# Optimization experiments

Measured on AMD Instinct MI355X. Metric: run time of the kernel, lower is better.

## Reference

```python
import jax, jax.numpy as jnp
import numpy as np

N = 8192
F_IN = 128
F_OUT = 64
NEG_INF = -9e15


def setup_inputs() -> dict:
    key = jax.random.key(0)
    k1, k2, k3, k4 = jax.random.split(key, 4)
    x = jax.random.normal(k1, (N, F_IN), dtype=jnp.float32)
    adj = jax.random.randint(k2, (N, N), 0, 2, dtype=jnp.int32)
    W = jax.random.normal(k3, (F_OUT, F_IN), dtype=jnp.float32) * 0.05  # torch Linear weight [out,in]
    a = jax.random.normal(k4, (1, 2 * F_OUT), dtype=jnp.float32) * 0.05  # attention vector weight [1, 2*out]
    return {"x": x, "adj": adj, "W": W, "a": a}


def reference(x, adj, W, a):
    fout = W.shape[0]
    Wh = x @ W.T                                   # [N, out]
    a1 = a[0, :fout]                               # a.weight.T[:out]
    a2 = a[0, fout:]                               # a.weight.T[out:]
    Wh1 = Wh @ a1                                  # [N]
    Wh2 = Wh @ a2                                  # [N]
    e = jax.nn.leaky_relu(Wh1[:, None] + Wh2[None, :], negative_slope=0.2)  # [N, N]
    attention = jnp.where(adj > 0, e, NEG_INF)
    attention = jax.nn.softmax(attention, axis=1)
    # dropout is identity in eval / deterministic reference
    h_prime = attention @ Wh                       # [N, out]
    return jax.nn.elu(h_prime)
```

## Files before the change

### kernel.cpp

```cpp
#include <hip/hip_runtime.h>
#include <cstdint>
#include <cstddef>

#define NN 8192
#define FIN 128
#define FOUT 64

typedef __attribute__((ext_vector_type(8))) short short8;
typedef __attribute__((ext_vector_type(4))) float f32x4;

__device__ __forceinline__ unsigned short f32_to_bf16_bits(float f) {
    union { float f; uint32_t u; } c; c.f = f;
    uint32_t u = c.u;
    u += 0x7fffu + ((u >> 16) & 1u);
    return (unsigned short)(u >> 16);
}

__device__ __forceinline__ unsigned int pack_bf16(float lo, float hi) {
    return (unsigned int)f32_to_bf16_bits(lo) |
           ((unsigned int)f32_to_bf16_bits(hi) << 16);
}

__global__ __launch_bounds__(256) void gat_prep(
    const float* __restrict__ x, const float* __restrict__ W,
    const float* __restrict__ a, unsigned short* __restrict__ WhT,
    float* __restrict__ Wh1, float* __restrict__ Wh2)
{
    const int t    = threadIdx.x;
    const int f    = t & 63;
    const int iloc = t >> 6;
    const int i    = blockIdx.x * 4 + iloc;

    const float4* x4 = (const float4*)(x + (size_t)i * FIN);
    const float4* w4 = (const float4*)(W + (size_t)f * FIN);

    float acc = 0.f;
#pragma unroll
    for (int k = 0; k < FIN / 4; ++k) {
        float4 xv = x4[k];
        float4 wv = w4[k];
        acc += xv.x * wv.x + xv.y * wv.y + xv.z * wv.z + xv.w * wv.w;
    }

    WhT[(size_t)f * NN + i] = f32_to_bf16_bits(acc);

    float r1 = acc * a[f];
    float r2 = acc * a[64 + f];
#pragma unroll
    for (int m = 1; m < 64; m <<= 1) {
        r1 += __shfl_xor(r1, m, 64);
        r2 += __shfl_xor(r2, m, 64);
    }
    if (f == 0) { Wh1[i] = r1; Wh2[i] = r2; }
}

__global__ __launch_bounds__(256, 4) void gat_attn(
    const int* __restrict__ adj, const unsigned short* __restrict__ WhT,
    const float* __restrict__ Wh1, const float* __restrict__ Wh2,
    float* __restrict__ Cpart, float* __restrict__ Tpart)
{
    __shared__ float lds_C[4][16][68];
    __shared__ float lds_tot[4][16];

    const int tid  = threadIdx.x;
    const int wave = tid >> 6;
    const int lane = tid & 63;
    const int il   = lane & 15;
    const int q    = lane >> 4;
    const int rt   = blockIdx.x >> 1;
    const int jh   = blockIdx.x & 1;
    const int i0   = rt * 16;
    const int i    = i0 + il;

    const float wh1   = Wh1[i];
    const int   jbase = jh * 4096 + wave * 32 + q * 8;
    const int* __restrict__ adjrow = adj + (size_t)i * NN;

    const short8* bp0 = (const short8*)(WhT + (size_t)(0  + il) * NN);
    const short8* bp1 = (const short8*)(WhT + (size_t)(16 + il) * NN);
    const short8* bp2 = (const short8*)(WhT + (size_t)(32 + il) * NN);
    const short8* bp3 = (const short8*)(WhT + (size_t)(48 + il) * NN);

    f32x4 acc0 = {0.f, 0.f, 0.f, 0.f};
    f32x4 acc1 = {0.f, 0.f, 0.f, 0.f};
    f32x4 acc2 = {0.f, 0.f, 0.f, 0.f};
    f32x4 acc3 = {0.f, 0.f, 0.f, 0.f};
    float tot = 0.f;

    int4   av0 = *(const int4*)(adjrow + jbase);
    int4   av1 = *(const int4*)(adjrow + jbase + 4);
    float4 w20 = *(const float4*)(Wh2 + jbase);
    float4 w21 = *(const float4*)(Wh2 + jbase + 4);
    int jb = jbase >> 3;
    short8 b0 = bp0[jb];
    short8 b1 = bp1[jb];
    short8 b2 = bp2[jb];
    short8 b3 = bp3[jb];

    for (int tt = 0; tt < 32; ++tt) {
        const int jn = jbase + (((tt + 1) & 31) << 7);
        const int4   nav0 = *(const int4*)(adjrow + jn);
        const int4   nav1 = *(const int4*)(adjrow + jn + 4);
        const float4 nw20 = *(const float4*)(Wh2 + jn);
        const float4 nw21 = *(const float4*)(Wh2 + jn + 4);
        const int jnb = jn >> 3;
        const short8 nb0 = bp0[jnb];
        const short8 nb1 = bp1[jnb];
        const short8 nb2 = bp2[jnb];
        const short8 nb3 = bp3[jnb];

        float wv[8];
#define CALC(idx, adjv, wh2v)                                          \
        {                                                              \
            float s = wh1 + (wh2v);                                    \
            float e = fmaxf(s, 0.2f * s);          \
            float v = ((adjv) > 0) ? __expf(e) : 0.f;                  \
            tot += v;                                                  \
            wv[idx] = v;                                               \
        }
        CALC(0, av0.x, w20.x) CALC(1, av0.y, w20.y)
        CALC(2, av0.z, w20.z) CALC(3, av0.w, w20.w)
        CALC(4, av1.x, w21.x) CALC(5, av1.y, w21.y)
        CALC(6, av1.z, w21.z) CALC(7, av1.w, w21.w)
#undef CALC

        union { short8 v; unsigned int u[4]; } af;
        af.u[0] = pack_bf16(wv[0], wv[1]);
        af.u[1] = pack_bf16(wv[2], wv[3]);
        af.u[2] = pack_bf16(wv[4], wv[5]);
        af.u[3] = pack_bf16(wv[6], wv[7]);

        acc0 = __builtin_amdgcn_mfma_f32_16x16x32_bf16(af.v, b0, acc0, 0, 0, 0);
        acc1 = __builtin_amdgcn_mfma_f32_16x16x32_bf16(af.v, b1, acc1, 0, 0, 0);
        acc2 = __builtin_amdgcn_mfma_f32_16x16x32_bf16(af.v, b2, acc2, 0, 0, 0);
        acc3 = __builtin_amdgcn_mfma_f32_16x16x32_bf16(af.v, b3, acc3, 0, 0, 0);

        av0 = nav0; av1 = nav1; w20 = nw20; w21 = nw21;
        b0 = nb0; b1 = nb1; b2 = nb2; b3 = nb3;
    }

    tot += __shfl_xor(tot, 16, 64);
    tot += __shfl_xor(tot, 32, 64);
    if (lane < 16) lds_tot[wave][lane] = tot;

#pragma unroll
    for (int r = 0; r < 4; ++r) {
        lds_C[wave][q * 4 + r][0 * 16 + il] = acc0[r];
        lds_C[wave][q * 4 + r][1 * 16 + il] = acc1[r];
        lds_C[wave][q * 4 + r][2 * 16 + il] = acc2[r];
        lds_C[wave][q * 4 + r][3 * 16 + il] = acc3[r];
    }
    __syncthreads();

#pragma unroll
    for (int e = 0; e < 4; ++e) {
        const int idx = e * 256 + tid;
        const int ii = idx >> 6;
        const int ff = idx & 63;
        float s = lds_C[0][ii][ff] + lds_C[1][ii][ff] +
                  lds_C[2][ii][ff] + lds_C[3][ii][ff];
        Cpart[((size_t)jh * NN + i0 + ii) * FOUT + ff] = s;
        if (ff == 0) {
            float ts = lds_tot[0][ii] + lds_tot[1][ii] +
                       lds_tot[2][ii] + lds_tot[3][ii];
            Tpart[(size_t)jh * NN + i0 + ii] = ts;
        }
    }
}

__global__ __launch_bounds__(256) void gat_combine(
    const float* __restrict__ Cpart, const float* __restrict__ Tpart,
    float* __restrict__ out)
{
    const int idx = blockIdx.x * 256 + threadIdx.x;
    const int i = idx >> 6;
    const float c = Cpart[idx] + Cpart[(size_t)NN * FOUT + idx];
    const float t = Tpart[i] + Tpart[NN + i];
    const float p = c / t;
    out[idx] = (p > 0.f) ? p : (__expf(p) - 1.f);
}

extern "C" void kernel_launch(void* const* d_in, const int* in_sizes, int n_in,
                              void* d_out, int out_size, void* d_ws, size_t ws_size,
                              hipStream_t stream) {
    const float* x   = (const float*)d_in[0];
    const int*   adj = (const int*)d_in[1];
    const float* W   = (const float*)d_in[2];
    const float* a   = (const float*)d_in[3];
    float* out = (float*)d_out;

    char* ws = (char*)d_ws;
    unsigned short* WhT = (unsigned short*)ws;
    float* Wh1   = (float*)(ws + (size_t)1048576);
    float* Wh2   = (float*)(ws + (size_t)1048576 + 32768);
    float* Cpart = (float*)(ws + (size_t)2097152);
    float* Tpart = (float*)(ws + (size_t)6291456);

    gat_prep<<<dim3(NN / 4), dim3(256), 0, stream>>>(x, W, a, WhT, Wh1, Wh2);
    gat_attn<<<dim3(NN / 16 * 2), dim3(256), 0, stream>>>(adj, WhT, Wh1, Wh2, Cpart, Tpart);
    gat_combine<<<dim3(NN * FOUT / 256), dim3(256), 0, stream>>>(Cpart, Tpart, out);
}
```

Baseline: 424.4 us.

## Fuse combine into attention kernel with 512-thread blocks and deeper adj prefetch

The attention kernel now uses 8 waves per 16-row tile covering the full neighbour range instead of splitting the j range across two blocks. This removes the partial-sum buffers and the separate combine kernel, since normalisation and ELU are applied in the epilogue. It also prefetches adj and Wh2 two iterations ahead, loads the WhT operands inside the iteration without prefetch, splits the running sum into two accumulators, and uses the HIP bf16 pack intrinsic. There are half as many blocks as before (512 of 512 threads), which lowers the parallelism available to hide adj memory latency on the dominant 256 MB read.

```diff
diff --git a/kernel.cpp b/kernel.cpp
--- a/kernel.cpp
+++ b/kernel.cpp
@@ -1,4 +1,5 @@
 #include <hip/hip_runtime.h>
+#include <hip/hip_bf16.h>
 #include <cstdint>
 #include <cstddef>
 
@@ -14,11 +15,6 @@
     uint32_t u = c.u;
     u += 0x7fffu + ((u >> 16) & 1u);
     return (unsigned short)(u >> 16);
-}
-
-__device__ __forceinline__ unsigned int pack_bf16(float lo, float hi) {
-    return (unsigned int)f32_to_bf16_bits(lo) |
-           ((unsigned int)f32_to_bf16_bits(hi) << 16);
 }
 
 __global__ __launch_bounds__(256) void gat_prep(
@@ -54,26 +50,24 @@
     if (f == 0) { Wh1[i] = r1; Wh2[i] = r2; }
 }
 
-__global__ __launch_bounds__(256, 4) void gat_attn(
+__global__ __launch_bounds__(512, 4) void gat_attn(
     const int* __restrict__ adj, const unsigned short* __restrict__ WhT,
     const float* __restrict__ Wh1, const float* __restrict__ Wh2,
-    float* __restrict__ Cpart, float* __restrict__ Tpart)
+    float* __restrict__ out)
 {
-    __shared__ float lds_C[4][16][68];
-    __shared__ float lds_tot[4][16];
+    __shared__ float lds_C[8][16][68];
+    __shared__ float lds_tot[8][16];
 
     const int tid  = threadIdx.x;
     const int wave = tid >> 6;
     const int lane = tid & 63;
     const int il   = lane & 15;
     const int q    = lane >> 4;
-    const int rt   = blockIdx.x >> 1;
-    const int jh   = blockIdx.x & 1;
-    const int i0   = rt * 16;
+    const int i0   = blockIdx.x * 16;
     const int i    = i0 + il;
 
     const float wh1   = Wh1[i];
-    const int   jbase = jh * 4096 + wave * 32 + q * 8;
+    const int   jbase = wave * 32 + q * 8;
     const int* __restrict__ adjrow = adj + (size_t)i * NN;
 
     const short8* bp0 = (const short8*)(WhT + (size_t)(0  + il) * NN);
@@ -85,60 +79,62 @@
     f32x4 acc1 = {0.f, 0.f, 0.f, 0.f};
     f32x4 acc2 = {0.f, 0.f, 0.f, 0.f};
     f32x4 acc3 = {0.f, 0.f, 0.f, 0.f};
-    float tot = 0.f;
+    float tot0 = 0.f, tot1 = 0.f;
 
-    int4   av0 = *(const int4*)(adjrow + jbase);
-    int4   av1 = *(const int4*)(adjrow + jbase + 4);
-    float4 w20 = *(const float4*)(Wh2 + jbase);
-    float4 w21 = *(const float4*)(Wh2 + jbase + 4);
-    int jb = jbase >> 3;
-    short8 b0 = bp0[jb];
-    short8 b1 = bp1[jb];
-    short8 b2 = bp2[jb];
-    short8 b3 = bp3[jb];
+    int4   aA0 = *(const int4*)(adjrow + jbase);
+    int4   aA1 = *(const int4*)(adjrow + jbase + 4);
+    float4 wA0 = *(const float4*)(Wh2 + jbase);
+    float4 wA1 = *(const float4*)(Wh2 + jbase + 4);
+    int4   aB0 = *(const int4*)(adjrow + jbase + 256);
+    int4   aB1 = *(const int4*)(adjrow + jbase + 260);
+    float4 wB0 = *(const float4*)(Wh2 + jbase + 256);
+    float4 wB1 = *(const float4*)(Wh2 + jbase + 260);
 
+#pragma unroll 4
     for (int tt = 0; tt < 32; ++tt) {
-        const int jn = jbase + (((tt + 1) & 31) << 7);
-        const int4   nav0 = *(const int4*)(adjrow + jn);
-        const int4   nav1 = *(const int4*)(adjrow + jn + 4);
-        const float4 nw20 = *(const float4*)(Wh2 + jn);
-        const float4 nw21 = *(const float4*)(Wh2 + jn + 4);
-        const int jnb = jn >> 3;
-        const short8 nb0 = bp0[jnb];
-        const short8 nb1 = bp1[jnb];
-        const short8 nb2 = bp2[jnb];
-        const short8 nb3 = bp3[jnb];
+        const int jb = (jbase + (tt << 8)) >> 3;
+        short8 b0 = bp0[jb];
+        short8 b1 = bp1[jb];
+        short8 b2 = bp2[jb];
+        short8 b3 = bp3[jb];
+
+        const int jn = jbase + (((tt + 2) & 31) << 8);
+        const int4   nA0 = *(const int4*)(adjrow + jn);
+        const int4   nA1 = *(const int4*)(adjrow + jn + 4);
+        const float4 nW0 = *(const float4*)(Wh2 + jn);
+        const float4 nW1 = *(const float4*)(Wh2 + jn + 4);
 
         float wv[8];
-#define CALC(idx, adjv, wh2v)                                          \
+#define CALC(idx, adjv, wh2v, totv)                                    \
         {                                                              \
             float s = wh1 + (wh2v);                                    \
             float e = fmaxf(s, 0.2f * s);          \
             float v = ((adjv) > 0) ? __expf(e) : 0.f;                  \
-            tot += v;                                                  \
+            totv += v;                                                 \
             wv[idx] = v;                                               \
         }
-        CALC(0, av0.x, w20.x) CALC(1, av0.y, w20.y)
-        CALC(2, av0.z, w20.z) CALC(3, av0.w, w20.w)
-        CALC(4, av1.x, w21.x) CALC(5, av1.y, w21.y)
-        CALC(6, av1.z, w21.z) CALC(7, av1.w, w21.w)
+        CALC(0, aA0.x, wA0.x, tot0) CALC(1, aA0.y, wA0.y, tot1)
+        CALC(2, aA0.z, wA0.z, tot0) CALC(3, aA0.w, wA0.w, tot1)
+        CALC(4, aA1.x, wA1.x, tot0) CALC(5, aA1.y, wA1.y, tot1)
+        CALC(6, aA1.z, wA1.z, tot0) CALC(7, aA1.w, wA1.w, tot1)
 #undef CALC
 
-        union { short8 v; unsigned int u[4]; } af;
-        af.u[0] = pack_bf16(wv[0], wv[1]);
-        af.u[1] = pack_bf16(wv[2], wv[3]);
-        af.u[2] = pack_bf16(wv[4], wv[5]);
-        af.u[3] = pack_bf16(wv[6], wv[7]);
+        union { short8 v; __hip_bfloat162 h[4]; } af;
+        af.h[0] = __float22bfloat162_rn(float2{wv[0], wv[1]});
+        af.h[1] = __float22bfloat162_rn(float2{wv[2], wv[3]});
+        af.h[2] = __float22bfloat162_rn(float2{wv[4], wv[5]});
+        af.h[3] = __float22bfloat162_rn(float2{wv[6], wv[7]});
 
         acc0 = __builtin_amdgcn_mfma_f32_16x16x32_bf16(af.v, b0, acc0, 0, 0, 0);
         acc1 = __builtin_amdgcn_mfma_f32_16x16x32_bf16(af.v, b1, acc1, 0, 0, 0);
         acc2 = __builtin_amdgcn_mfma_f32_16x16x32_bf16(af.v, b2, acc2, 0, 0, 0);
         acc3 = __builtin_amdgcn_mfma_f32_16x16x32_bf16(af.v, b3, acc3, 0, 0, 0);
 
-        av0 = nav0; av1 = nav1; w20 = nw20; w21 = nw21;
-        b0 = nb0; b1 = nb1; b2 = nb2; b3 = nb3;
+        aA0 = aB0; aA1 = aB1; wA0 = wB0; wA1 = wB1;
+        aB0 = nA0; aB1 = nA1; wB0 = nW0; wB1 = nW1;
     }
 
+    float tot = tot0 + tot1;
     tot += __shfl_xor(tot, 16, 64);
     tot += __shfl_xor(tot, 32, 64);
     if (lane < 16) lds_tot[wave][lane] = tot;
@@ -153,31 +149,19 @@
     __syncthreads();
 
 #pragma unroll
-    for (int e = 0; e < 4; ++e) {
-        const int idx = e * 256 + tid;
+    for (int e = 0; e < 2; ++e) {
+        const int idx = e * 512 + tid;
         const int ii = idx >> 6;
         const int ff = idx & 63;
-        float s = lds_C[0][ii][ff] + lds_C[1][ii][ff] +
-                  lds_C[2][ii][ff] + lds_C[3][ii][ff];
-        Cpart[((size_t)jh * NN + i0 + ii) * FOUT + ff] = s;
-        if (ff == 0) {
-            float ts = lds_tot[0][ii] + lds_tot[1][ii] +
-                       lds_tot[2][ii] + lds_tot[3][ii];
-            Tpart[(size_t)jh * NN + i0 + ii] = ts;
-        }
+        float s = 0.f;
+#pragma unroll
+        for (int w = 0; w < 8; ++w) s += lds_C[w][ii][ff];
+        float t = lds_tot[0][ii] + lds_tot[1][ii] + lds_tot[2][ii] +
+                  lds_tot[3][ii] + lds_tot[4][ii] + lds_tot[5][ii] +
+                  lds_tot[6][ii] + lds_tot[7][ii];
+        const float p = s / t;
+        out[(size_t)(i0 + ii) * FOUT + ff] = (p > 0.f) ? p : (__expf(p) - 1.f);
     }
-}
-
-__global__ __launch_bounds__(256) void gat_combine(
-    const float* __restrict__ Cpart, const float* __restrict__ Tpart,
-    float* __restrict__ out)
-{
-    const int idx = blockIdx.x * 256 + threadIdx.x;
-    const int i = idx >> 6;
-    const float c = Cpart[idx] + Cpart[(size_t)NN * FOUT + idx];
-    const float t = Tpart[i] + Tpart[NN + i];
-    const float p = c / t;
-    out[idx] = (p > 0.f) ? p : (__expf(p) - 1.f);
 }
 
 extern "C" void kernel_launch(void* const* d_in, const int* in_sizes, int n_in,
@@ -193,10 +177,7 @@
     unsigned short* WhT = (unsigned short*)ws;
     float* Wh1   = (float*)(ws + (size_t)1048576);
     float* Wh2   = (float*)(ws + (size_t)1048576 + 32768);
-    float* Cpart = (float*)(ws + (size_t)2097152);
-    float* Tpart = (float*)(ws + (size_t)6291456);
 
     gat_prep<<<dim3(NN / 4), dim3(256), 0, stream>>>(x, W, a, WhT, Wh1, Wh2);
-    gat_attn<<<dim3(NN / 16 * 2), dim3(256), 0, stream>>>(adj, WhT, Wh1, Wh2, Cpart, Tpart);
-    gat_combine<<<dim3(NN * FOUT / 256), dim3(256), 0, stream>>>(Cpart, Tpart, out);
+    gat_attn<<<dim3(NN / 16), dim3(512), 0, stream>>>(adj, WhT, Wh1, Wh2, out);
 }
```

Measured after the change: 451.9 us. 6.5% more time.
